# Kernel optimization log

Measured on AMD Instinct MI355X. Metric: run time of the kernel, lower is better.

## Reference

```python
import jax, jax.numpy as jnp
import numpy as np

H = 256
H2 = H // 2
N = 1024
T = 12
B = 4


def setup_inputs() -> dict:
    key = jax.random.key(0)
    ks = jax.random.split(key, 12)
    s = lambda fan_in: 1.0 / np.sqrt(fan_in)
    inp = {
        "node_embeddings": jax.random.normal(ks[0], (B, N, H), jnp.float32),
        # origin encoder: Linear(H,H) -> ReLU -> Linear(H,H2)
        "W1o": jax.random.normal(ks[1], (H, H), jnp.float32) * s(H),
        "b1o": jnp.zeros((H,), jnp.float32),
        "W2o": jax.random.normal(ks[2], (H, H2), jnp.float32) * s(H),
        "b2o": jnp.zeros((H2,), jnp.float32),
        # dest encoder
        "W1d": jax.random.normal(ks[3], (H, H), jnp.float32) * s(H),
        "b1d": jnp.zeros((H,), jnp.float32),
        "W2d": jax.random.normal(ks[4], (H, H2), jnp.float32) * s(H),
        "b2d": jnp.zeros((H2,), jnp.float32),
        # bilinear: out = o @ Wb @ d^T + bb  (torch nn.Bilinear(H2,H2,1))
        "Wb": jax.random.normal(ks[5], (H2, H2), jnp.float32) * s(H2),
        "bb": jnp.zeros((), jnp.float32),
        # horizon predictor: Linear(1, T) -> ReLU
        "wh": jax.random.normal(ks[6], (T,), jnp.float32),
        "bh": jnp.zeros((T,), jnp.float32),
    }
    return inp


def reference(node_embeddings, W1o, b1o, W2o, b2o, W1d, b1d, W2d, b2d, Wb, bb, wh, bh):
    # encoders (dropout is identity at eval)
    o = jax.nn.relu(node_embeddings @ W1o + b1o) @ W2o + b2o      # (B,N,H2)
    d = jax.nn.relu(node_embeddings @ W1d + b1d) @ W2d + b2d      # (B,N,H2)
    # bilinear score without materializing (B,N,N,H2):
    oW = jnp.einsum("bik,kl->bil", o, Wb)                          # (B,N,H2)
    scores = jnp.einsum("bil,bjl->bij", oW, d) + bb                # (B,N,N)
    # horizon predictor Linear(1,T)+ReLU, then permute to (B,T,N,N)
    pred = jax.nn.relu(scores[..., None] * wh + bh)                # (B,N,N,T)
    pred = jnp.transpose(pred, (0, 3, 1, 2))                       # (B,T,N,N)
    return jax.nn.relu(pred)
```

## Files before the change

### kernel.cpp

```cpp
#include <hip/hip_runtime.h>
#include <hip/hip_bf16.h>

constexpr int H  = 256;
constexpr int H2 = 128;
constexpr int N  = 1024;
constexpr int T  = 12;
constexpr int B  = 4;
constexpr int M  = B * N;

using short8 = __attribute__((ext_vector_type(8))) short;
using f32x4  = __attribute__((ext_vector_type(4))) float;

__device__ __forceinline__ unsigned short f2bf(float f) {
    union { float f; unsigned int u; } v; v.f = f;
    unsigned int u = v.u;
    u += 0x7FFFu + ((u >> 16) & 1u);
    return (unsigned short)(u >> 16);
}

__global__ void fold_wb_kernel(const float* __restrict__ W2o,
                               const float* __restrict__ b2o,
                               const float* __restrict__ Wb,
                               float* __restrict__ W2of,
                               float* __restrict__ b2of) {
    __shared__ float row[H2];
    const int i = blockIdx.x;
    const int j = threadIdx.x;
    const float* src = (i < H) ? (W2o + i * H2) : b2o;
    row[j] = src[j];
    __syncthreads();
    float acc = 0.f;
#pragma unroll 8
    for (int k = 0; k < H2; ++k) acc = fmaf(row[k], Wb[k * H2 + j], acc);
    if (i < H) W2of[i * H2 + j] = acc;
    else       b2of[j] = acc;
}

__global__ void prep_kernel(const float* __restrict__ x,
                            const float* __restrict__ W1o, const float* __restrict__ W1d,
                            const float* __restrict__ b1o, const float* __restrict__ b1d,
                            const float* __restrict__ W2of, const float* __restrict__ b2of,
                            const float* __restrict__ W2d,  const float* __restrict__ b2d,
                            unsigned short* __restrict__ xb,
                            unsigned short* __restrict__ W1T,
                            unsigned short* __restrict__ W2T,
                            float* __restrict__ bias1, float* __restrict__ bias2)
{
    const int NX  = M * H;
    const int NW1 = 512 * H;
    const int NW2 = 256 * H;
    const int TOT = NX + NW1 + NW2 + 512 + 256;
    for (int i = blockIdx.x * blockDim.x + threadIdx.x; i < TOT;
         i += gridDim.x * blockDim.x) {
        if (i < NX) {
            xb[i] = f2bf(x[i]);
        } else if (i < NX + NW1) {
            const int j = i - NX, n = j >> 8, k = j & 255;
            const float v = (n < 256) ? W1o[k * H + n] : W1d[k * H + (n - 256)];
            W1T[j] = f2bf(v);
        } else if (i < NX + NW1 + NW2) {
            const int j = i - NX - NW1, n = j >> 8, k = j & 255;
            const float v = (n < 128) ? W2of[k * H2 + n] : W2d[k * H2 + (n - 128)];
            W2T[j] = f2bf(v);
        } else if (i < NX + NW1 + NW2 + 512) {
            const int j = i - NX - NW1 - NW2;
            bias1[j] = (j < 256) ? b1o[j] : b1d[j - 256];
        } else {
            const int j = i - NX - NW1 - NW2 - 512;
            bias2[j] = (j < 128) ? b2of[j] : b2d[j - 128];
        }
    }
}

template<bool RELU>
__device__ __forceinline__ void enc_body(
    const unsigned short* __restrict__ A, int lda,
    const unsigned short* __restrict__ Bt,
    const float* __restrict__ bias,
    unsigned short* __restrict__ C, int ldc)
{
    __shared__ unsigned short Abuf[64 * 40];
    __shared__ unsigned short Bbuf[64 * 40];
    const int tid = threadIdx.x;
    const int w  = tid >> 6;
    const int l  = tid & 63;
    const int lr = tid >> 2;
    const int lk = (tid & 3) * 8;

    uint4 aR = *(const uint4*)(A + (size_t)lr * lda + lk);
    uint4 bR = *(const uint4*)(Bt + (size_t)lr * 256 + lk);

    f32x4 z = {0.f, 0.f, 0.f, 0.f};
    f32x4 acc[4] = {z, z, z, z};

    for (int kc = 0; kc < 256; kc += 32) {
        if (kc) __syncthreads();
        *(uint4*)&Abuf[lr * 40 + lk] = aR;
        *(uint4*)&Bbuf[lr * 40 + lk] = bR;
        __syncthreads();
        if (kc + 32 < 256) {
            aR = *(const uint4*)(A + (size_t)lr * lda + kc + 32 + lk);
            bR = *(const uint4*)(Bt + (size_t)lr * 256 + kc + 32 + lk);
        }
        const int q8 = (l >> 4) * 8;
        const short8 bf = *(const short8*)&Bbuf[(w * 16 + (l & 15)) * 40 + q8];
#pragma unroll
        for (int it = 0; it < 4; ++it) {
            const short8 af = *(const short8*)&Abuf[(it * 16 + (l & 15)) * 40 + q8];
            acc[it] = __builtin_amdgcn_mfma_f32_16x16x32_bf16(af, bf, acc[it], 0, 0, 0);
        }
    }

    const int n  = w * 16 + (l & 15);
    const int r0 = (l >> 4) * 4;
    const float bn = bias[n];
#pragma unroll
    for (int it = 0; it < 4; ++it)
#pragma unroll
        for (int r = 0; r < 4; ++r) {
            float v = acc[it][r] + bn;
            if (RELU) v = fmaxf(v, 0.f);
            C[(size_t)(it * 16 + r0 + r) * ldc + n] = f2bf(v);
        }
}

__global__ __launch_bounds__(256) void enc1_kernel(
    const unsigned short* __restrict__ xb, const unsigned short* __restrict__ W1T,
    const float* __restrict__ bias1, unsigned short* __restrict__ h)
{
    const int bx = blockIdx.x, by = blockIdx.y;
    enc_body<true>(xb + (size_t)by * 64 * 256, 256,
                   W1T + (size_t)bx * 64 * 256,
                   bias1 + bx * 64,
                   h + (size_t)by * 64 * 512 + bx * 64, 512);
}

__global__ __launch_bounds__(256) void enc2_kernel(
    const unsigned short* __restrict__ h, const unsigned short* __restrict__ W2T,
    const float* __restrict__ bias2, unsigned short* __restrict__ od)
{
    const int bx = blockIdx.x, by = blockIdx.y;
    enc_body<false>(h + (size_t)by * 64 * 512 + (bx >> 1) * 256, 512,
                    W2T + (size_t)bx * 64 * 256,
                    bias2 + bx * 64,
                    od + (size_t)by * 64 * 256 + bx * 64, 256);
}

__global__ __launch_bounds__(256) void k3_kernel(
    const unsigned short* __restrict__ od,
    const float* __restrict__ bbp, const float* __restrict__ wh,
    const float* __restrict__ bh, float* __restrict__ out)
{
    __shared__ unsigned short Abuf[64 * 40];
    __shared__ unsigned short Bbuf[64 * 40];
    const int tid = threadIdx.x;
    const int w  = tid >> 6;
    const int l  = tid & 63;
    const int lr = tid >> 2;
    const int lk = (tid & 3) * 8;
    const int b  = blockIdx.z;
    const int i0 = blockIdx.y * 64;
    const int j0 = blockIdx.x * 64;
    const unsigned short* Ab = od + ((size_t)b * N + i0) * 256;
    const unsigned short* Bb = od + ((size_t)b * N + j0) * 256 + 128;

    uint4 aR = *(const uint4*)(Ab + (size_t)lr * 256 + lk);
    uint4 bR = *(const uint4*)(Bb + (size_t)lr * 256 + lk);

    f32x4 z = {0.f, 0.f, 0.f, 0.f};
    f32x4 acc[4] = {z, z, z, z};

    for (int kc = 0; kc < H2; kc += 32) {
        if (kc) __syncthreads();
        *(uint4*)&Abuf[lr * 40 + lk] = aR;
        *(uint4*)&Bbuf[lr * 40 + lk] = bR;
        __syncthreads();
        if (kc + 32 < H2) {
            aR = *(const uint4*)(Ab + (size_t)lr * 256 + kc + 32 + lk);
            bR = *(const uint4*)(Bb + (size_t)lr * 256 + kc + 32 + lk);
        }
        const int q8 = (l >> 4) * 8;
        const short8 bf = *(const short8*)&Bbuf[(w * 16 + (l & 15)) * 40 + q8];
#pragma unroll
        for (int it = 0; it < 4; ++it) {
            const short8 af = *(const short8*)&Abuf[(it * 16 + (l & 15)) * 40 + q8];
            acc[it] = __builtin_amdgcn_mfma_f32_16x16x32_bf16(af, bf, acc[it], 0, 0, 0);
        }
    }

    const float bbv = bbp[0];
    float s[4][4];
#pragma unroll
    for (int it = 0; it < 4; ++it)
#pragma unroll
        for (int r = 0; r < 4; ++r) s[it][r] = acc[it][r] + bbv;

    const int jcol = j0 + w * 16 + (l & 15);
    const int r0   = (l >> 4) * 4;
#pragma unroll
    for (int t = 0; t < T; ++t) {
        const float wt = wh[t], bt = bh[t];
        float* ob = out + ((size_t)(b * T + t) * N + i0 + r0) * N + jcol;
#pragma unroll
        for (int it = 0; it < 4; ++it)
#pragma unroll
            for (int r = 0; r < 4; ++r)
                ob[(size_t)(it * 16 + r) * N] = fmaxf(fmaf(s[it][r], wt, bt), 0.f);
    }
}

extern "C" void kernel_launch(void* const* d_in, const int* in_sizes, int n_in,
                              void* d_out, int out_size, void* d_ws, size_t ws_size,
                              hipStream_t stream) {
    const float* x   = (const float*)d_in[0];
    const float* W1o = (const float*)d_in[1];
    const float* b1o = (const float*)d_in[2];
    const float* W2o = (const float*)d_in[3];
    const float* b2o = (const float*)d_in[4];
    const float* W1d = (const float*)d_in[5];
    const float* b1d = (const float*)d_in[6];
    const float* W2d = (const float*)d_in[7];
    const float* b2d = (const float*)d_in[8];
    const float* Wb  = (const float*)d_in[9];
    const float* bb  = (const float*)d_in[10];
    const float* wh  = (const float*)d_in[11];
    const float* bh  = (const float*)d_in[12];
    float* out = (float*)d_out;

    float* W2of  = (float*)d_ws;
    float* b2of  = W2of + H * H2;
    float* bias1 = b2of + H2;
    float* bias2 = bias1 + 512;
    unsigned short* xb  = (unsigned short*)(bias2 + 256);
    unsigned short* W1T = xb + (size_t)M * H;
    unsigned short* W2T = W1T + 512 * H;
    unsigned short* h   = W2T + 256 * H;
    unsigned short* od  = h + (size_t)M * 512;

    fold_wb_kernel<<<H + 1, H2, 0, stream>>>(W2o, b2o, Wb, W2of, b2of);

    prep_kernel<<<1024, 256, 0, stream>>>(x, W1o, W1d, b1o, b1d,
                                          W2of, b2of, W2d, b2d,
                                          xb, W1T, W2T, bias1, bias2);

    enc1_kernel<<<dim3(8, M / 64), 256, 0, stream>>>(xb, W1T, bias1, h);

    enc2_kernel<<<dim3(4, M / 64), 256, 0, stream>>>(h, W2T, bias2, od);

    k3_kernel<<<dim3(N / 64, N / 64, B), 256, 0, stream>>>(od, bb, wh, bh, out);
}
```

Before: 250.7 us.

## Fuse weight folding into prep, convert x to bf16 inside enc1, nontemporal output stores

Merges the Wb-folding kernel into the weight-prep kernel, which now writes the transposed bf16 W2T directly, and removes one launch. The fp32-to-bf16 conversion of the input activations moves into the enc1 GEMM load path, so the separate full pass over x and the xb buffer are gone. The large output writes in the score kernel become nontemporal stores to reduce cache pollution. The cost is that enc1 reads twice as many bytes per A tile and does the packing work inline.

```diff
diff --git a/kernel.cpp b/kernel.cpp
--- a/kernel.cpp
+++ b/kernel.cpp
@@ -18,66 +18,58 @@
     return (unsigned short)(u >> 16);
 }
 
-__global__ void fold_wb_kernel(const float* __restrict__ W2o,
-                               const float* __restrict__ b2o,
-                               const float* __restrict__ Wb,
-                               float* __restrict__ W2of,
-                               float* __restrict__ b2of) {
-    __shared__ float row[H2];
-    const int i = blockIdx.x;
-    const int j = threadIdx.x;
-    const float* src = (i < H) ? (W2o + i * H2) : b2o;
-    row[j] = src[j];
-    __syncthreads();
-    float acc = 0.f;
+__device__ __forceinline__ uint4 pack8(const float4& f0, const float4& f1) {
+    union { unsigned short u[8]; uint4 v; } r;
+    r.u[0] = f2bf(f0.x); r.u[1] = f2bf(f0.y); r.u[2] = f2bf(f0.z); r.u[3] = f2bf(f0.w);
+    r.u[4] = f2bf(f1.x); r.u[5] = f2bf(f1.y); r.u[6] = f2bf(f1.z); r.u[7] = f2bf(f1.w);
+    return r.v;
+}
+
+__global__ __launch_bounds__(256) void prep_kernel(
+    const float* __restrict__ W1o, const float* __restrict__ b1o,
+    const float* __restrict__ W2o, const float* __restrict__ b2o,
+    const float* __restrict__ W1d, const float* __restrict__ b1d,
+    const float* __restrict__ W2d, const float* __restrict__ b2d,
+    const float* __restrict__ Wb,
+    unsigned short* __restrict__ W1T, unsigned short* __restrict__ W2T,
+    float* __restrict__ bias1, float* __restrict__ bias2)
+{
+    const int bx = blockIdx.x;
+    const int t  = threadIdx.x;
+    if (bx < 256) {
+        __shared__ float row[H2];
+        if (t < H2) row[t] = W2o[bx * H2 + t];
+        __syncthreads();
+        if (t < H2) {
+            float acc = 0.f;
 #pragma unroll 8
-    for (int k = 0; k < H2; ++k) acc = fmaf(row[k], Wb[k * H2 + j], acc);
-    if (i < H) W2of[i * H2 + j] = acc;
-    else       b2of[j] = acc;
-}
-
-__global__ void prep_kernel(const float* __restrict__ x,
-                            const float* __restrict__ W1o, const float* __restrict__ W1d,
-                            const float* __restrict__ b1o, const float* __restrict__ b1d,
-                            const float* __restrict__ W2of, const float* __restrict__ b2of,
-                            const float* __restrict__ W2d,  const float* __restrict__ b2d,
-                            unsigned short* __restrict__ xb,
-                            unsigned short* __restrict__ W1T,
-                            unsigned short* __restrict__ W2T,
-                            float* __restrict__ bias1, float* __restrict__ bias2)
-{
-    const int NX  = M * H;
-    const int NW1 = 512 * H;
-    const int NW2 = 256 * H;
-    const int TOT = NX + NW1 + NW2 + 512 + 256;
-    for (int i = blockIdx.x * blockDim.x + threadIdx.x; i < TOT;
-         i += gridDim.x * blockDim.x) {
-        if (i < NX) {
-            xb[i] = f2bf(x[i]);
-        } else if (i < NX + NW1) {
-            const int j = i - NX, n = j >> 8, k = j & 255;
-            const float v = (n < 256) ? W1o[k * H + n] : W1d[k * H + (n - 256)];
-            W1T[j] = f2bf(v);
-        } else if (i < NX + NW1 + NW2) {
-            const int j = i - NX - NW1, n = j >> 8, k = j & 255;
-            const float v = (n < 128) ? W2of[k * H2 + n] : W2d[k * H2 + (n - 128)];
-            W2T[j] = f2bf(v);
-        } else if (i < NX + NW1 + NW2 + 512) {
-            const int j = i - NX - NW1 - NW2;
-            bias1[j] = (j < 256) ? b1o[j] : b1d[j - 256];
+            for (int l = 0; l < H2; ++l) acc = fmaf(row[l], Wb[l * H2 + t], acc);
+            W2T[t * H + bx] = f2bf(acc);
+        }
+    } else if (bx == 256) {
+        bias1[t]       = b1o[t];
+        bias1[256 + t] = b1d[t];
+        if (t < H2) {
+            float acc = 0.f;
+#pragma unroll 8
+            for (int l = 0; l < H2; ++l) acc = fmaf(b2o[l], Wb[l * H2 + t], acc);
+            bias2[t] = acc;
         } else {
-            const int j = i - NX - NW1 - NW2 - 512;
-            bias2[j] = (j < 128) ? b2of[j] : b2d[j - 128];
-        }
-    }
-}
-
-template<bool RELU>
-__device__ __forceinline__ void enc_body(
-    const unsigned short* __restrict__ A, int lda,
-    const unsigned short* __restrict__ Bt,
-    const float* __restrict__ bias,
-    unsigned short* __restrict__ C, int ldc)
+            bias2[t] = b2d[t - H2];
+        }
+    } else if (bx < 769) {
+        const int n = bx - 257;
+        const float v = (n < 256) ? W1o[t * H + n] : W1d[t * H + (n - 256)];
+        W1T[n * H + t] = f2bf(v);
+    } else {
+        const int m = bx - 769;
+        W2T[(128 + m) * H + t] = f2bf(W2d[t * H2 + m]);
+    }
+}
+
+__global__ __launch_bounds__(256) void enc1_kernel(
+    const float* __restrict__ x, const unsigned short* __restrict__ W1T,
+    const float* __restrict__ bias1, unsigned short* __restrict__ h)
 {
     __shared__ unsigned short Abuf[64 * 40];
     __shared__ unsigned short Bbuf[64 * 40];
@@ -87,20 +79,80 @@
     const int lr = tid >> 2;
     const int lk = (tid & 3) * 8;
 
-    uint4 aR = *(const uint4*)(A + (size_t)lr * lda + lk);
-    uint4 bR = *(const uint4*)(Bt + (size_t)lr * 256 + lk);
+    const float* A = x + ((size_t)blockIdx.y * 64) * H;
+    const unsigned short* Bt = W1T + (size_t)blockIdx.x * 64 * H;
+    const float* bias = bias1 + blockIdx.x * 64;
+    unsigned short* C = h + ((size_t)blockIdx.y * 64) * 512 + blockIdx.x * 64;
+
+    float4 a0 = *(const float4*)(A + (size_t)lr * H + lk);
+    float4 a1 = *(const float4*)(A + (size_t)lr * H + lk + 4);
+    uint4  bR = *(const uint4*)(Bt + (size_t)lr * H + lk);
 
     f32x4 z = {0.f, 0.f, 0.f, 0.f};
     f32x4 acc[4] = {z, z, z, z};
 
-    for (int kc = 0; kc < 256; kc += 32) {
+    for (int kc = 0; kc < H; kc += 32) {
+        if (kc) __syncthreads();
+        *(uint4*)&Abuf[lr * 40 + lk] = pack8(a0, a1);
+        *(uint4*)&Bbuf[lr * 40 + lk] = bR;
+        __syncthreads();
+        if (kc + 32 < H) {
+            a0 = *(const float4*)(A + (size_t)lr * H + kc + 32 + lk);
+            a1 = *(const float4*)(A + (size_t)lr * H + kc + 32 + lk + 4);
+            bR = *(const uint4*)(Bt + (size_t)lr * H + kc + 32 + lk);
+        }
+        const int q8 = (l >> 4) * 8;
+        const short8 bf = *(const short8*)&Bbuf[(w * 16 + (l & 15)) * 40 + q8];
+#pragma unroll
+        for (int it = 0; it < 4; ++it) {
+            const short8 af = *(const short8*)&Abuf[(it * 16 + (l & 15)) * 40 + q8];
+            acc[it] = __builtin_amdgcn_mfma_f32_16x16x32_bf16(af, bf, acc[it], 0, 0, 0);
+        }
+    }
+
+    const int n  = w * 16 + (l & 15);
+    const int r0 = (l >> 4) * 4;
+    const float bn = bias[n];
+#pragma unroll
+    for (int it = 0; it < 4; ++it)
+#pragma unroll
+        for (int r = 0; r < 4; ++r)
+            C[(size_t)(it * 16 + r0 + r) * 512 + n] =
+                f2bf(fmaxf(acc[it][r] + bn, 0.f));
+}
+
+__global__ __launch_bounds__(256) void enc2_kernel(
+    const unsigned short* __restrict__ h, const unsigned short* __restrict__ W2T,
+    const float* __restrict__ bias2, unsigned short* __restrict__ od)
+{
+    __shared__ unsigned short Abuf[64 * 40];
+    __shared__ unsigned short Bbuf[64 * 40];
+    const int tid = threadIdx.x;
+    const int w  = tid >> 6;
+    const int l  = tid & 63;
+    const int lr = tid >> 2;
+    const int lk = (tid & 3) * 8;
+    const int bx = blockIdx.x;
+
+    const unsigned short* A  = h + ((size_t)blockIdx.y * 64) * 512 + (bx >> 1) * 256;
+    const unsigned short* Bt = W2T + (size_t)bx * 64 * H;
+    const float* bias = bias2 + bx * 64;
+    unsigned short* C = od + ((size_t)blockIdx.y * 64) * 256 + bx * 64;
+
+    uint4 aR = *(const uint4*)(A + (size_t)lr * 512 + lk);
+    uint4 bR = *(const uint4*)(Bt + (size_t)lr * H + lk);
+
+    f32x4 z = {0.f, 0.f, 0.f, 0.f};
+    f32x4 acc[4] = {z, z, z, z};
+
+    for (int kc = 0; kc < H; kc += 32) {
         if (kc) __syncthreads();
         *(uint4*)&Abuf[lr * 40 + lk] = aR;
         *(uint4*)&Bbuf[lr * 40 + lk] = bR;
         __syncthreads();
-        if (kc + 32 < 256) {
-            aR = *(const uint4*)(A + (size_t)lr * lda + kc + 32 + lk);
-            bR = *(const uint4*)(Bt + (size_t)lr * 256 + kc + 32 + lk);
+        if (kc + 32 < H) {
+            aR = *(const uint4*)(A + (size_t)lr * 512 + kc + 32 + lk);
+            bR = *(const uint4*)(Bt + (size_t)lr * H + kc + 32 + lk);
         }
         const int q8 = (l >> 4) * 8;
         const short8 bf = *(const short8*)&Bbuf[(w * 16 + (l & 15)) * 40 + q8];
@@ -117,33 +169,8 @@
 #pragma unroll
     for (int it = 0; it < 4; ++it)
 #pragma unroll
-        for (int r = 0; r < 4; ++r) {
-            float v = acc[it][r] + bn;
-            if (RELU) v = fmaxf(v, 0.f);
-            C[(size_t)(it * 16 + r0 + r) * ldc + n] = f2bf(v);
-        }
-}
-
-__global__ __launch_bounds__(256) void enc1_kernel(
-    const unsigned short* __restrict__ xb, const unsigned short* __restrict__ W1T,
-    const float* __restrict__ bias1, unsigned short* __restrict__ h)
-{
-    const int bx = blockIdx.x, by = blockIdx.y;
-    enc_body<true>(xb + (size_t)by * 64 * 256, 256,
-                   W1T + (size_t)bx * 64 * 256,
-                   bias1 + bx * 64,
-                   h + (size_t)by * 64 * 512 + bx * 64, 512);
-}
-
-__global__ __launch_bounds__(256) void enc2_kernel(
-    const unsigned short* __restrict__ h, const unsigned short* __restrict__ W2T,
-    const float* __restrict__ bias2, unsigned short* __restrict__ od)
-{
-    const int bx = blockIdx.x, by = blockIdx.y;
-    enc_body<false>(h + (size_t)by * 64 * 512 + (bx >> 1) * 256, 512,
-                    W2T + (size_t)bx * 64 * 256,
-                    bias2 + bx * 64,
-                    od + (size_t)by * 64 * 256 + bx * 64, 256);
+        for (int r = 0; r < 4; ++r)
+            C[(size_t)(it * 16 + r0 + r) * 256 + n] = f2bf(acc[it][r] + bn);
 }
 
 __global__ __launch_bounds__(256) void k3_kernel(
@@ -205,7 +232,9 @@
         for (int it = 0; it < 4; ++it)
 #pragma unroll
             for (int r = 0; r < 4; ++r)
-                ob[(size_t)(it * 16 + r) * N] = fmaxf(fmaf(s[it][r], wt, bt), 0.f);
+                __builtin_nontemporal_store(
+                    fmaxf(fmaf(s[it][r], wt, bt), 0.f),
+                    ob + (size_t)(it * 16 + r) * N);
     }
 }
 
@@ -227,23 +256,17 @@
     const float* bh  = (const float*)d_in[12];
     float* out = (float*)d_out;
 
-    float* W2of  = (float*)d_ws;
-    float* b2of  = W2of + H * H2;
-    float* bias1 = b2of + H2;
+    float* bias1 = (float*)d_ws;
     float* bias2 = bias1 + 512;
-    unsigned short* xb  = (unsigned short*)(bias2 + 256);
-    unsigned short* W1T = xb + (size_t)M * H;
+    unsigned short* W1T = (unsigned short*)(bias2 + 256);
     unsigned short* W2T = W1T + 512 * H;
     unsigned short* h   = W2T + 256 * H;
     unsigned short* od  = h + (size_t)M * 512;
 
-    fold_wb_kernel<<<H + 1, H2, 0, stream>>>(W2o, b2o, Wb, W2of, b2of);
-
-    prep_kernel<<<1024, 256, 0, stream>>>(x, W1o, W1d, b1o, b1d,
-                                          W2of, b2of, W2d, b2d,
-                                          xb, W1T, W2T, bias1, bias2);
-
-    enc1_kernel<<<dim3(8, M / 64), 256, 0, stream>>>(xb, W1T, bias1, h);
+    prep_kernel<<<897, 256, 0, stream>>>(W1o, b1o, W2o, b2o, W1d, b1d,
+                                         W2d, b2d, Wb, W1T, W2T, bias1, bias2);
+
+    enc1_kernel<<<dim3(8, M / 64), 256, 0, stream>>>(x, W1T, bias1, h);
 
     enc2_kernel<<<dim3(4, M / 64), 256, 0, stream>>>(h, W2T, bias2, od);
 
```

After: 272.5 us. +8.7%, slower.
